# Performance work log

Hardware: AMD Instinct MI355X
Metric: run time of the kernel (lower is better)

Reference implementation:

```python
import jax, jax.numpy as jnp
import numpy as np

B, L, D_MODEL = 2, 1024, 1024
D_STATE, D_CONV, EXPAND = 16, 4, 2
D_INNER = D_MODEL * EXPAND
LN_EPS = 1e-5


def setup_inputs() -> dict:
    key = jax.random.key(0)
    ks = jax.random.split(key, 6)
    g = lambda k, shape, scale: (jax.random.normal(k, shape, jnp.float32) * scale)
    x = jax.random.normal(ks[0], (B, L, D_MODEL), jnp.float32)
    in_proj_w = g(ks[1], (2 * D_INNER, D_MODEL), D_MODEL ** -0.5)
    conv_w = g(ks[2], (D_INNER, D_CONV), D_CONV ** -0.5)   # depthwise kernel
    conv_b = jnp.zeros((D_INNER,), jnp.float32)
    x_proj_w = g(ks[3], (2 * D_STATE + 1, D_INNER), D_INNER ** -0.5)
    A_log = jnp.tile(jnp.log(jnp.arange(1, D_STATE + 1, dtype=jnp.float32)), (D_INNER, 1))
    D_param = jnp.ones((D_INNER,), jnp.float32)
    dt_w = g(ks[4], (D_INNER, 1), 1.0)
    dt_b = jnp.full((D_INNER,), -4.0, jnp.float32)
    out_w = g(ks[5], (D_MODEL, D_INNER), D_INNER ** -0.5)
    ln_g = jnp.ones((D_INNER,), jnp.float32)
    ln_b = jnp.zeros((D_INNER,), jnp.float32)
    return dict(x=x, in_proj_w=in_proj_w, conv_w=conv_w, conv_b=conv_b,
                x_proj_w=x_proj_w, A_log=A_log, D_param=D_param,
                dt_w=dt_w, dt_b=dt_b, out_w=out_w, ln_g=ln_g, ln_b=ln_b)


def _forward(x, in_proj_w, conv_w, conv_b, x_proj_w, A_log, D_param,
             dt_w, dt_b, out_w, ln_g, ln_b):
    Lq = x.shape[1]
    xz = jnp.einsum('bld,ed->ble', x, in_proj_w)            # (B,L,2*Di)
    xb, z = xz[..., :D_INNER], xz[..., D_INNER:]
    # causal depthwise conv1d (pad left d_conv-1, valid conv == torch pad+truncate)
    xpad = jnp.pad(xb, ((0, 0), (D_CONV - 1, 0), (0, 0)))
    xc = conv_b
    for k in range(D_CONV):
        xc = xc + xpad[:, k:k + Lq, :] * conv_w[:, k]
    xb = jax.nn.silu(xc)
    proj = jnp.einsum('bld,ed->ble', xb, x_proj_w)          # (B,L,2N+1)
    dt_in = proj[..., :1]
    Bp = proj[..., 1:1 + D_STATE]                            # (B,L,N)
    Cp = proj[..., 1 + D_STATE:]                             # (B,L,N)
    dt = jax.nn.softplus(dt_in * dt_w[:, 0] + dt_b)          # (B,L,Di)
    A = -jnp.exp(A_log)                                      # (Di,N)
    dA = jnp.exp(dt[..., None] * A)                          # (B,L,Di,N)
    x_scaled = (xb * dt)[..., None] * Bp[..., None, :]       # (B,L,Di,N)
    # linear recurrence h[t] = dA[t]*h[t-1] + x_scaled[t] via associative scan
    def comb(a, b):
        return (a[0] * b[0], b[0] * a[1] + b[1])
    _, h = jax.lax.associative_scan(comb, (dA, x_scaled), axis=1)
    y = jnp.einsum('bldn,bln->bld', h, Cp) + xb * D_param    # (B,L,Di)
    mu = jnp.mean(y, axis=-1, keepdims=True)
    var = jnp.var(y, axis=-1, keepdims=True)
    y = (y - mu) / jnp.sqrt(var + LN_EPS) * ln_g + ln_b
    y = y * jax.nn.silu(z)
    return jnp.einsum('bld,ed->ble', y, out_w)               # (B,L,d_model)


def reference(x, in_proj_w, conv_w, conv_b, x_proj_w, A_log, D_param,
              dt_w, dt_b, out_w, ln_g, ln_b):
    return _forward(x, in_proj_w, conv_w, conv_b, x_proj_w, A_log, D_param,
                    dt_w, dt_b, out_w, ln_g, ln_b)
```

## Files before the change

### kernel.cpp

```cpp
#include <hip/hip_runtime.h>

typedef unsigned short u16;
typedef unsigned int u32;
typedef __bf16 bf16x8 __attribute__((ext_vector_type(8)));
typedef float f32x4 __attribute__((ext_vector_type(4)));

__device__ __forceinline__ float bf2f(u16 b) {
    return __uint_as_float(((u32)b) << 16);
}
__device__ __forceinline__ u16 f2bf(float f) {
    u32 u = __float_as_uint(f);
    return (u16)((u + 0x7fffu + ((u >> 16) & 1u)) >> 16);
}

#define P_CONVW 0
#define P_CONVB 8192
#define P_ALOG  10240
#define P_DPAR  43008
#define P_DTW   45056
#define P_DTB   47104
#define P_LNG   49152
#define P_LNB   51200
#define P_TOTAL 53248

#define CCH 32
#define CT  32
#define CHUNKTOT 2097152
#define PSTRIDE 128

struct ParamPtrs { const void* p[8]; };

__global__ __launch_bounds__(256) void canon_params(ParamPtrs pp, float* __restrict__ dst,
                                                    const u16* __restrict__ dp) {
    const bool isbf = (dp[0] != 0);
    const int i = blockIdx.x * 256 + threadIdx.x;
    int seg, off;
    if (i < P_CONVB)      { seg = 0; off = i; }
    else if (i < P_ALOG)  { seg = 1; off = i - P_CONVB; }
    else if (i < P_DPAR)  { seg = 2; off = i - P_ALOG; }
    else if (i < P_DTW)   { seg = 3; off = i - P_DPAR; }
    else if (i < P_DTB)   { seg = 4; off = i - P_DTW; }
    else if (i < P_LNG)   { seg = 5; off = i - P_DTB; }
    else if (i < P_LNB)   { seg = 6; off = i - P_LNG; }
    else                  { seg = 7; off = i - P_LNB; }
    dst[i] = isbf ? bf2f(((const u16*)pp.p[seg])[off]) : ((const float*)pp.p[seg])[off];
}

#define CV_X   524288
#define CV_W1  1572864
#define CV_TOT 2097152
__global__ __launch_bounds__(256) void canon_multi(const void* __restrict__ sx,
                                                   const void* __restrict__ sw1,
                                                   const void* __restrict__ swo,
                                                   u16* __restrict__ dst,
                                                   const u16* __restrict__ dp) {
    const bool isbf = (dp[0] != 0);
    const int i = blockIdx.x * 256 + threadIdx.x;
    if (i >= CV_TOT) return;
    const void* src;
    int off;
    if (i < CV_X)       { src = sx;  off = i; }
    else if (i < CV_W1) { src = sw1; off = i - CV_X; }
    else                { src = swo; off = i - CV_W1; }
    if (isbf) {
        ((uint2*)dst)[i] = ((const uint2*)src)[off];
    } else {
        const float4 v = ((const float4*)src)[off];
        uint2 o;
        o.x = (u32)f2bf(v.x) | ((u32)f2bf(v.y) << 16);
        o.y = (u32)f2bf(v.z) | ((u32)f2bf(v.w) << 16);
        ((uint2*)dst)[i] = o;
    }
}

__global__ __launch_bounds__(256) void canon_wpad(const void* __restrict__ src,
                                                  u16* __restrict__ dst,
                                                  const u16* __restrict__ dp) {
    const bool isbf = (dp[0] != 0);
    const int i = blockIdx.x * 256 + threadIdx.x;
    const int idx = i * 4;
    const int row = idx >> 11;
    u16 o[4];
#pragma unroll
    for (int q = 0; q < 4; ++q) {
        float v = 0.f;
        if (row < 33)
            v = isbf ? bf2f(((const u16*)src)[idx + q]) : ((const float*)src)[idx + q];
        o[q] = f2bf(v);
    }
    *(uint2*)&dst[idx] = *(uint2*)o;
}

template <bool STORE_F32>
__global__ __launch_bounds__(256) void gemm_bt(const u16* __restrict__ A,
                                               const u16* __restrict__ Bw,
                                               void* __restrict__ C,
                                               int M, int N, int Kseg,
                                               int lda, int ldb) {
    const int bm = blockIdx.x;
    const int bn = blockIdx.y;
    const int kbase = blockIdx.z * Kseg;
    const int tid = threadIdx.x;
    const int lane = tid & 63;
    const int wave = tid >> 6;
    const int wm = wave >> 1, wn = wave & 1;
    const int l16 = lane & 15, quad = lane >> 4;

    __shared__ __align__(16) u16 sA[128 * 32];
    __shared__ __align__(16) u16 sB[128 * 32];

    f32x4 acc[4][4] = {};

    const int rsub = lane >> 2;
    const int csub = (lane & 3) * 8;

    for (int k0 = 0; k0 < Kseg; k0 += 32) {
        const int kc = kbase + k0 + csub;
        __syncthreads();
#pragma unroll
        for (int q = 0; q < 2; ++q) {
            const int g = wave + 4 * q;
            const int row = g * 16 + rsub;
            __builtin_amdgcn_global_load_lds(
                (const u32*)&A[(size_t)(bm * 128 + row) * lda + kc],
                (u32*)&sA[g * 512], 16, 0, 0);
            __builtin_amdgcn_global_load_lds(
                (const u32*)&Bw[(size_t)(bn * 128 + row) * ldb + kc],
                (u32*)&sB[g * 512], 16, 0, 0);
        }
        __syncthreads();

        bf16x8 af[4], bg[4];
#pragma unroll
        for (int t = 0; t < 4; ++t) {
            af[t] = *(const bf16x8*)&sA[(wm * 64 + t * 16 + l16) * 32 + quad * 8];
            bg[t] = *(const bf16x8*)&sB[(wn * 64 + t * 16 + l16) * 32 + quad * 8];
        }
#pragma unroll
        for (int mt = 0; mt < 4; ++mt)
#pragma unroll
            for (int nt = 0; nt < 4; ++nt)
                acc[mt][nt] = __builtin_amdgcn_mfma_f32_16x16x32_bf16(
                    af[mt], bg[nt], acc[mt][nt], 0, 0, 0);
    }

    float* Cf = (float*)C + (size_t)blockIdx.z * M * N;
#pragma unroll
    for (int mt = 0; mt < 4; ++mt) {
#pragma unroll
        for (int r = 0; r < 4; ++r) {
            const int row = bm * 128 + wm * 64 + mt * 16 + quad * 4 + r;
#pragma unroll
            for (int nt = 0; nt < 4; ++nt) {
                const int col = bn * 128 + wn * 64 + nt * 16 + l16;
                if (STORE_F32)
                    Cf[(size_t)row * N + col] = acc[mt][nt][r];
                else
                    ((u16*)C)[(size_t)row * N + col] = f2bf(acc[mt][nt][r]);
            }
        }
    }
}

__global__ __launch_bounds__(256) void reduce_parts(const float* __restrict__ src,
                                                    float* __restrict__ dst,
                                                    int n4, int parts) {
    const int i = blockIdx.x * 256 + threadIdx.x;
    if (i >= n4) return;
    float4 s = ((const float4*)src)[i];
    for (int p = 1; p < parts; ++p) {
        const float4 v = ((const float4*)src)[(size_t)p * n4 + i];
        s.x += v.x; s.y += v.y; s.z += v.z; s.w += v.w;
    }
    ((float4*)dst)[i] = s;
}

__global__ __launch_bounds__(256) void conv_silu(const u16* __restrict__ xz,
                                                 const float* __restrict__ par,
                                                 u16* __restrict__ xb16) {
    const int idx = blockIdx.x * 256 + threadIdx.x;
    const int d = idx & 2047;
    const int bl = idx >> 11;
    const int l = bl & 1023;
    float acc = par[P_CONVB + d];
#pragma unroll
    for (int k = 0; k < 4; ++k) {
        const int ls = l + k - 3;
        if (ls >= 0)
            acc = fmaf(bf2f(xz[(size_t)(bl + (ls - l)) * 4096 + d]),
                       par[P_CONVW + d * 4 + k], acc);
    }
    const float s = acc / (1.f + __expf(-acc));
    xb16[idx] = f2bf(s);
}

__global__ __launch_bounds__(256) void scan_p1(const u16* __restrict__ xb16,
                                               const float* __restrict__ proj,
                                               const float* __restrict__ par,
                                               float* __restrict__ PS) {
    const int d = blockIdx.x * 256 + threadIdx.x;
    const int c = blockIdx.y;
    const int b = blockIdx.z;
    __shared__ float sp[CT][33];
    const size_t row0 = (size_t)b * 1024 + c * CT;
    for (int f = threadIdx.x; f < CT * 33; f += 256) {
        const int i = f / 33, j = f - i * 33;
        sp[i][j] = proj[(row0 + i) * PSTRIDE + j];
    }
    float Aneg[16];
#pragma unroll
    for (int n = 0; n < 16; ++n) Aneg[n] = -__expf(par[P_ALOG + d * 16 + n]);
    const float dtw = par[P_DTW + d], dtb = par[P_DTB + d];
    __syncthreads();

    float h[16] = {}, P[16];
#pragma unroll
    for (int n = 0; n < 16; ++n) P[n] = 1.f;

    float xv = bf2f(xb16[row0 * 2048 + d]);
    for (int i = 0; i < CT; ++i) {
        const float xv_next = (i + 1 < CT) ? bf2f(xb16[(row0 + i + 1) * 2048 + d]) : 0.f;
        const float dtin = sp[i][0];
        const float darg = fmaf(dtin, dtw, dtb);
        const float dt = (darg > 20.f) ? darg : __logf(1.f + __expf(darg));
        const float xdt = xv * dt;
#pragma unroll
        for (int n = 0; n < 16; ++n) {
            const float dA = __expf(dt * Aneg[n]);
            P[n] *= dA;
            h[n] = fmaf(dA, h[n], xdt * sp[i][1 + n]);
        }
        xv = xv_next;
    }
    const size_t base = (((size_t)b * CCH + c) * 16) * 2048 + d;
#pragma unroll
    for (int n = 0; n < 16; ++n) {
        PS[base + (size_t)n * 2048] = P[n];
        PS[CHUNKTOT + base + (size_t)n * 2048] = h[n];
    }
}

__global__ __launch_bounds__(256) void scan_comb(const float* __restrict__ PS,
                                                 float* __restrict__ H) {
    const int t = blockIdx.x * 256 + threadIdx.x;
    const int d = t & 2047;
    const int n = (t >> 11) & 15;
    const int b = t >> 15;
    float h = 0.f;
#pragma unroll
    for (int c = 0; c < CCH; ++c) {
        const size_t idx = (((size_t)b * CCH + c) * 16 + n) * 2048 + d;
        H[idx] = h;
        h = fmaf(PS[idx], h, PS[CHUNKTOT + idx]);
    }
}

__global__ __launch_bounds__(256) void scan_p2(const u16* __restrict__ xb16,
                                               const float* __restrict__ proj,
                                               const float* __restrict__ par,
                                               const float* __restrict__ H,
                                               u16* __restrict__ y) {
    const int d = blockIdx.x * 256 + threadIdx.x;
    const int c = blockIdx.y;
    const int b = blockIdx.z;
    __shared__ float sp[CT][33];
    const size_t row0 = (size_t)b * 1024 + c * CT;
    for (int f = threadIdx.x; f < CT * 33; f += 256) {
        const int i = f / 33, j = f - i * 33;
        sp[i][j] = proj[(row0 + i) * PSTRIDE + j];
    }
    float Aneg[16], h[16];
    const size_t hbase = (((size_t)b * CCH + c) * 16) * 2048 + d;
#pragma unroll
    for (int n = 0; n < 16; ++n) {
        Aneg[n] = -__expf(par[P_ALOG + d * 16 + n]);
        h[n] = H[hbase + (size_t)n * 2048];
    }
    const float dtw = par[P_DTW + d], dtb = par[P_DTB + d];
    const float Dp = par[P_DPAR + d];
    __syncthreads();

    float xv = bf2f(xb16[row0 * 2048 + d]);
    for (int i = 0; i < CT; ++i) {
        const float xv_next = (i + 1 < CT) ? bf2f(xb16[(row0 + i + 1) * 2048 + d]) : 0.f;
        const float dtin = sp[i][0];
        const float darg = fmaf(dtin, dtw, dtb);
        const float dt = (darg > 20.f) ? darg : __logf(1.f + __expf(darg));
        const float xdt = xv * dt;
        float acc = 0.f;
#pragma unroll
        for (int n = 0; n < 16; ++n) {
            const float dA = __expf(dt * Aneg[n]);
            h[n] = fmaf(dA, h[n], xdt * sp[i][1 + n]);
            acc = fmaf(h[n], sp[i][17 + n], acc);
        }
        y[(row0 + i) * 2048 + d] = f2bf(fmaf(xv, Dp, acc));
        xv = xv_next;
    }
}

__global__ __launch_bounds__(256) void ln_silu(const u16* __restrict__ y,
                                               const u16* __restrict__ xz,
                                               const float* __restrict__ par,
                                               u16* __restrict__ yn) {
    const int row = blockIdx.x;
    const int tid = threadIdx.x;
    const int lane = tid & 63, wave = tid >> 6;
    float v[8];
    float s = 0.f, s2 = 0.f;
#pragma unroll
    for (int i = 0; i < 8; ++i) {
        v[i] = bf2f(y[(size_t)row * 2048 + tid + i * 256]);
        s += v[i];
        s2 = fmaf(v[i], v[i], s2);
    }
    s += __shfl_xor(s, 1); s2 += __shfl_xor(s2, 1);
    s += __shfl_xor(s, 2); s2 += __shfl_xor(s2, 2);
    s += __shfl_xor(s, 4); s2 += __shfl_xor(s2, 4);
    s += __shfl_xor(s, 8); s2 += __shfl_xor(s2, 8);
    s += __shfl_xor(s, 16); s2 += __shfl_xor(s2, 16);
    s += __shfl_xor(s, 32); s2 += __shfl_xor(s2, 32);
    __shared__ float rs[4], rs2[4];
    if (lane == 0) { rs[wave] = s; rs2[wave] = s2; }
    __syncthreads();
    const float ts = rs[0] + rs[1] + rs[2] + rs[3];
    const float ts2 = rs2[0] + rs2[1] + rs2[2] + rs2[3];
    const float mu = ts * (1.f / 2048.f);
    const float var = ts2 * (1.f / 2048.f) - mu * mu;
    const float rstd = rsqrtf(var + 1e-5f);
#pragma unroll
    for (int i = 0; i < 8; ++i) {
        const int d = tid + i * 256;
        float t = (v[i] - mu) * rstd * par[P_LNG + d] + par[P_LNB + d];
        const float z = bf2f(xz[(size_t)row * 4096 + 2048 + d]);
        t *= z / (1.f + __expf(-z));
        yn[(size_t)row * 2048 + d] = f2bf(t);
    }
}

extern "C" void kernel_launch(void* const* d_in, const int* in_sizes, int n_in,
                              void* d_out, int out_size, void* d_ws, size_t ws_size,
                              hipStream_t stream) {
    const void* x         = d_in[0];
    const void* in_proj_w = d_in[1];
    const void* conv_w    = d_in[2];
    const void* conv_b    = d_in[3];
    const void* x_proj_w  = d_in[4];
    const void* A_log     = d_in[5];
    const void* D_param   = d_in[6];
    const void* dt_w      = d_in[7];
    const void* dt_b      = d_in[8];
    const void* out_w     = d_in[9];
    const void* ln_g      = d_in[10];
    const void* ln_b      = d_in[11];
    const u16* dp = (const u16*)D_param;

    float* cpar = (float*)d_ws;
    u16* cx     = (u16*)(cpar + P_TOTAL);
    u16* cw1    = cx + 2097152;
    u16* cwo    = cw1 + 4194304;
    u16* xz     = cwo + 2097152;
    u16* xb16   = xz + 8388608;
    u16* y      = xb16 + 4194304;
    u16* wpad   = y + 4194304;
    float* proj = (float*)(wpad + 262144);
    float* PS   = proj + 262144;
    float* H    = PS + 2 * CHUNKTOT;
    float* xpart = (float*)cx;
    float* gpart = PS;
    u16* yn      = xb16;

    ParamPtrs pp;
    pp.p[0] = conv_w; pp.p[1] = conv_b; pp.p[2] = A_log; pp.p[3] = D_param;
    pp.p[4] = dt_w;   pp.p[5] = dt_b;   pp.p[6] = ln_g;  pp.p[7] = ln_b;
    canon_params<<<P_TOTAL / 256, 256, 0, stream>>>(pp, cpar, dp);
    canon_multi<<<CV_TOT / 256, 256, 0, stream>>>(x, in_proj_w, out_w, cx, dp);
    canon_wpad<<<256, 256, 0, stream>>>(x_proj_w, wpad, dp);

    gemm_bt<false><<<dim3(16, 32, 1), 256, 0, stream>>>(cx, cw1, xz, 2048, 4096, 1024, 1024, 1024);
    conv_silu<<<16384, 256, 0, stream>>>(xz, cpar, xb16);
    gemm_bt<true><<<dim3(16, 1, 8), 256, 0, stream>>>(xb16, wpad, xpart, 2048, 128, 256, 2048, 2048);
    reduce_parts<<<256, 256, 0, stream>>>(xpart, proj, 65536, 8);
    scan_p1<<<dim3(8, CCH, 2), 256, 0, stream>>>(xb16, proj, cpar, PS);
    scan_comb<<<256, 256, 0, stream>>>(PS, H);
    scan_p2<<<dim3(8, CCH, 2), 256, 0, stream>>>(xb16, proj, cpar, H, y);
    ln_silu<<<2048, 256, 0, stream>>>(y, xz, cpar, yn);
    gemm_bt<true><<<dim3(16, 8, 2), 256, 0, stream>>>(yn, cwo, gpart, 2048, 1024, 1024, 2048, 2048);
    reduce_parts<<<2048, 256, 0, stream>>>(gpart, (float*)d_out, 524288, 2);
}
```

Measured before the change: 256.3 us.

## Merge canon kernels, replace split-K reductions with atomics, vectorize conv and layernorm

Folds the three input-canonicalisation kernels into one launch, which also zero-fills the projection buffer and the output. Both split-K GEMMs now accumulate through float atomic adds, which removes the two reduce_parts passes and their partial-sum buffers. The conv+SiLU and LN+SiLU kernels are rewritten to process 8 channels per thread with 128-bit loads and stores. This cuts launches and memory traffic, but atomic accumulation makes the floating-point summation order nondeterministic.

New measurement: 255.4 us. Within noise of the previous version (-0.3%).

```diff
diff --git a/kernel.cpp b/kernel.cpp
--- a/kernel.cpp
+++ b/kernel.cpp
@@ -4,6 +4,7 @@
 typedef unsigned int u32;
 typedef __bf16 bf16x8 __attribute__((ext_vector_type(8)));
 typedef float f32x4 __attribute__((ext_vector_type(4)));
+typedef unsigned short ushort8 __attribute__((ext_vector_type(8)));
 
 __device__ __forceinline__ float bf2f(u16 b) {
     return __uint_as_float(((u32)b) << 16);
@@ -28,70 +29,76 @@
 #define CHUNKTOT 2097152
 #define PSTRIDE 128
 
-struct ParamPtrs { const void* p[8]; };
-
-__global__ __launch_bounds__(256) void canon_params(ParamPtrs pp, float* __restrict__ dst,
-                                                    const u16* __restrict__ dp) {
-    const bool isbf = (dp[0] != 0);
-    const int i = blockIdx.x * 256 + threadIdx.x;
-    int seg, off;
-    if (i < P_CONVB)      { seg = 0; off = i; }
-    else if (i < P_ALOG)  { seg = 1; off = i - P_CONVB; }
-    else if (i < P_DPAR)  { seg = 2; off = i - P_ALOG; }
-    else if (i < P_DTW)   { seg = 3; off = i - P_DPAR; }
-    else if (i < P_DTB)   { seg = 4; off = i - P_DTW; }
-    else if (i < P_LNG)   { seg = 5; off = i - P_DTB; }
-    else if (i < P_LNB)   { seg = 6; off = i - P_LNG; }
-    else                  { seg = 7; off = i - P_LNB; }
-    dst[i] = isbf ? bf2f(((const u16*)pp.p[seg])[off]) : ((const float*)pp.p[seg])[off];
-}
-
 #define CV_X   524288
 #define CV_W1  1572864
 #define CV_TOT 2097152
-__global__ __launch_bounds__(256) void canon_multi(const void* __restrict__ sx,
-                                                   const void* __restrict__ sw1,
-                                                   const void* __restrict__ swo,
-                                                   u16* __restrict__ dst,
-                                                   const u16* __restrict__ dp) {
+
+struct ParamPtrs { const void* p[8]; };
+
+__global__ __launch_bounds__(256) void canon_all(ParamPtrs pp, float* __restrict__ cpar,
+                                                 const void* __restrict__ sx,
+                                                 const void* __restrict__ sw1,
+                                                 const void* __restrict__ swo,
+                                                 u16* __restrict__ cx,
+                                                 const void* __restrict__ sxp,
+                                                 u16* __restrict__ wpad,
+                                                 float* __restrict__ proj,
+                                                 float* __restrict__ dout,
+                                                 const u16* __restrict__ dp) {
     const bool isbf = (dp[0] != 0);
-    const int i = blockIdx.x * 256 + threadIdx.x;
-    if (i >= CV_TOT) return;
-    const void* src;
-    int off;
-    if (i < CV_X)       { src = sx;  off = i; }
-    else if (i < CV_W1) { src = sw1; off = i - CV_X; }
-    else                { src = swo; off = i - CV_W1; }
-    if (isbf) {
-        ((uint2*)dst)[i] = ((const uint2*)src)[off];
+    const int blk = blockIdx.x;
+    const int tid = threadIdx.x;
+    if (blk < 8192) {
+        const int i = blk * 256 + tid;
+        const void* src;
+        int off;
+        if (i < CV_X)       { src = sx;  off = i; }
+        else if (i < CV_W1) { src = sw1; off = i - CV_X; }
+        else                { src = swo; off = i - CV_W1; }
+        if (isbf) {
+            ((uint2*)cx)[i] = ((const uint2*)src)[off];
+        } else {
+            const float4 v = ((const float4*)src)[off];
+            uint2 o;
+            o.x = (u32)f2bf(v.x) | ((u32)f2bf(v.y) << 16);
+            o.y = (u32)f2bf(v.z) | ((u32)f2bf(v.w) << 16);
+            ((uint2*)cx)[i] = o;
+        }
+    } else if (blk < 8400) {
+        const int i = (blk - 8192) * 256 + tid;
+        int seg, off;
+        if (i < P_CONVB)      { seg = 0; off = i; }
+        else if (i < P_ALOG)  { seg = 1; off = i - P_CONVB; }
+        else if (i < P_DPAR)  { seg = 2; off = i - P_ALOG; }
+        else if (i < P_DTW)   { seg = 3; off = i - P_DPAR; }
+        else if (i < P_DTB)   { seg = 4; off = i - P_DTW; }
+        else if (i < P_LNG)   { seg = 5; off = i - P_DTB; }
+        else if (i < P_LNB)   { seg = 6; off = i - P_LNG; }
+        else                  { seg = 7; off = i - P_LNB; }
+        cpar[i] = isbf ? bf2f(((const u16*)pp.p[seg])[off]) : ((const float*)pp.p[seg])[off];
+    } else if (blk < 8656) {
+        const int i = (blk - 8400) * 256 + tid;
+        const int idx = i * 4;
+        const int row = idx >> 11;
+        u16 o[4];
+#pragma unroll
+        for (int q = 0; q < 4; ++q) {
+            float v = 0.f;
+            if (row < 33)
+                v = isbf ? bf2f(((const u16*)sxp)[idx + q]) : ((const float*)sxp)[idx + q];
+            o[q] = f2bf(v);
+        }
+        *(uint2*)&wpad[idx] = *(uint2*)o;
+    } else if (blk < 8912) {
+        const int i = (blk - 8656) * 256 + tid;
+        ((float4*)proj)[i] = make_float4(0.f, 0.f, 0.f, 0.f);
     } else {
-        const float4 v = ((const float4*)src)[off];
-        uint2 o;
-        o.x = (u32)f2bf(v.x) | ((u32)f2bf(v.y) << 16);
-        o.y = (u32)f2bf(v.z) | ((u32)f2bf(v.w) << 16);
-        ((uint2*)dst)[i] = o;
-    }
-}
-
-__global__ __launch_bounds__(256) void canon_wpad(const void* __restrict__ src,
-                                                  u16* __restrict__ dst,
-                                                  const u16* __restrict__ dp) {
-    const bool isbf = (dp[0] != 0);
-    const int i = blockIdx.x * 256 + threadIdx.x;
-    const int idx = i * 4;
-    const int row = idx >> 11;
-    u16 o[4];
-#pragma unroll
-    for (int q = 0; q < 4; ++q) {
-        float v = 0.f;
-        if (row < 33)
-            v = isbf ? bf2f(((const u16*)src)[idx + q]) : ((const float*)src)[idx + q];
-        o[q] = f2bf(v);
-    }
-    *(uint2*)&dst[idx] = *(uint2*)o;
-}
-
-template <bool STORE_F32>
+        const int i = (blk - 8912) * 256 + tid;
+        ((float4*)dout)[i] = make_float4(0.f, 0.f, 0.f, 0.f);
+    }
+}
+
+template <int MODE>
 __global__ __launch_bounds__(256) void gemm_bt(const u16* __restrict__ A,
                                                const u16* __restrict__ Bw,
                                                void* __restrict__ C,
@@ -144,7 +151,7 @@
                     af[mt], bg[nt], acc[mt][nt], 0, 0, 0);
     }
 
-    float* Cf = (float*)C + (size_t)blockIdx.z * M * N;
+    float* Cf = (float*)C + (MODE == 1 ? (size_t)blockIdx.z * M * N : (size_t)0);
 #pragma unroll
     for (int mt = 0; mt < 4; ++mt) {
 #pragma unroll
@@ -153,45 +160,56 @@
 #pragma unroll
             for (int nt = 0; nt < 4; ++nt) {
                 const int col = bn * 128 + wn * 64 + nt * 16 + l16;
-                if (STORE_F32)
+                if (MODE == 0)
+                    ((u16*)C)[(size_t)row * N + col] = f2bf(acc[mt][nt][r]);
+                else if (MODE == 1)
                     Cf[(size_t)row * N + col] = acc[mt][nt][r];
                 else
-                    ((u16*)C)[(size_t)row * N + col] = f2bf(acc[mt][nt][r]);
+                    unsafeAtomicAdd(&Cf[(size_t)row * N + col], acc[mt][nt][r]);
             }
         }
     }
-}
-
-__global__ __launch_bounds__(256) void reduce_parts(const float* __restrict__ src,
-                                                    float* __restrict__ dst,
-                                                    int n4, int parts) {
-    const int i = blockIdx.x * 256 + threadIdx.x;
-    if (i >= n4) return;
-    float4 s = ((const float4*)src)[i];
-    for (int p = 1; p < parts; ++p) {
-        const float4 v = ((const float4*)src)[(size_t)p * n4 + i];
-        s.x += v.x; s.y += v.y; s.z += v.z; s.w += v.w;
-    }
-    ((float4*)dst)[i] = s;
 }
 
 __global__ __launch_bounds__(256) void conv_silu(const u16* __restrict__ xz,
                                                  const float* __restrict__ par,
                                                  u16* __restrict__ xb16) {
     const int idx = blockIdx.x * 256 + threadIdx.x;
-    const int d = idx & 2047;
-    const int bl = idx >> 11;
+    const int d8 = idx & 255;
+    const int bl = idx >> 8;
     const int l = bl & 1023;
-    float acc = par[P_CONVB + d];
+    const int d0 = d8 * 8;
+
+    float acc[8];
+    {
+        const float4 b0 = *(const float4*)&par[P_CONVB + d0];
+        const float4 b1 = *(const float4*)&par[P_CONVB + d0 + 4];
+        acc[0] = b0.x; acc[1] = b0.y; acc[2] = b0.z; acc[3] = b0.w;
+        acc[4] = b1.x; acc[5] = b1.y; acc[6] = b1.z; acc[7] = b1.w;
+    }
+    float warr[8][4];
+#pragma unroll
+    for (int q = 0; q < 8; ++q) {
+        const float4 w = *(const float4*)&par[P_CONVW + (d0 + q) * 4];
+        warr[q][0] = w.x; warr[q][1] = w.y; warr[q][2] = w.z; warr[q][3] = w.w;
+    }
 #pragma unroll
     for (int k = 0; k < 4; ++k) {
         const int ls = l + k - 3;
-        if (ls >= 0)
-            acc = fmaf(bf2f(xz[(size_t)(bl + (ls - l)) * 4096 + d]),
-                       par[P_CONVW + d * 4 + k], acc);
-    }
-    const float s = acc / (1.f + __expf(-acc));
-    xb16[idx] = f2bf(s);
+        if (ls >= 0) {
+            const ushort8 xv = *(const ushort8*)&xz[(size_t)(bl + k - 3) * 4096 + d0];
+#pragma unroll
+            for (int q = 0; q < 8; ++q)
+                acc[q] = fmaf(bf2f(xv[q]), warr[q][k], acc[q]);
+        }
+    }
+    u16 o[8];
+#pragma unroll
+    for (int q = 0; q < 8; ++q) {
+        const float s = acc[q] / (1.f + __expf(-acc[q]));
+        o[q] = f2bf(s);
+    }
+    *(uint4*)&xb16[(size_t)bl * 2048 + d0] = *(uint4*)o;
 }
 
 __global__ __launch_bounds__(256) void scan_p1(const u16* __restrict__ xb16,
@@ -306,11 +324,13 @@
     const int row = blockIdx.x;
     const int tid = threadIdx.x;
     const int lane = tid & 63, wave = tid >> 6;
+    const int d0 = tid * 8;
+    const ushort8 vy = *(const ushort8*)&y[(size_t)row * 2048 + d0];
     float v[8];
     float s = 0.f, s2 = 0.f;
 #pragma unroll
     for (int i = 0; i < 8; ++i) {
-        v[i] = bf2f(y[(size_t)row * 2048 + tid + i * 256]);
+        v[i] = bf2f(vy[i]);
         s += v[i];
         s2 = fmaf(v[i], v[i], s2);
     }
@@ -328,14 +348,28 @@
     const float mu = ts * (1.f / 2048.f);
     const float var = ts2 * (1.f / 2048.f) - mu * mu;
     const float rstd = rsqrtf(var + 1e-5f);
+
+    const ushort8 vz = *(const ushort8*)&xz[(size_t)row * 4096 + 2048 + d0];
+    float g[8], bb[8];
+    {
+        const float4 g0 = *(const float4*)&par[P_LNG + d0];
+        const float4 g1 = *(const float4*)&par[P_LNG + d0 + 4];
+        g[0] = g0.x; g[1] = g0.y; g[2] = g0.z; g[3] = g0.w;
+        g[4] = g1.x; g[5] = g1.y; g[6] = g1.z; g[7] = g1.w;
+        const float4 b0 = *(const float4*)&par[P_LNB + d0];
+        const float4 b1 = *(const float4*)&par[P_LNB + d0 + 4];
+        bb[0] = b0.x; bb[1] = b0.y; bb[2] = b0.z; bb[3] = b0.w;
+        bb[4] = b1.x; bb[5] = b1.y; bb[6] = b1.z; bb[7] = b1.w;
+    }
+    u16 o[8];
 #pragma unroll
     for (int i = 0; i < 8; ++i) {
-        const int d = tid + i * 256;
-        float t = (v[i] - mu) * rstd * par[P_LNG + d] + par[P_LNB + d];
-        const float z = bf2f(xz[(size_t)row * 4096 + 2048 + d]);
+        float t = (v[i] - mu) * rstd * g[i] + bb[i];
+        const float z = bf2f(vz[i]);
         t *= z / (1.f + __expf(-z));
-        yn[(size_t)row * 2048 + d] = f2bf(t);
-    }
+        o[i] = f2bf(t);
+    }
+    *(uint4*)&yn[(size_t)row * 2048 + d0] = *(uint4*)o;
 }
 
 extern "C" void kernel_launch(void* const* d_in, const int* in_sizes, int n_in,
@@ -366,25 +400,20 @@
     float* proj = (float*)(wpad + 262144);
     float* PS   = proj + 262144;
     float* H    = PS + 2 * CHUNKTOT;
-    float* xpart = (float*)cx;
-    float* gpart = PS;
-    u16* yn      = xb16;
+    u16* yn     = xb16;
 
     ParamPtrs pp;
     pp.p[0] = conv_w; pp.p[1] = conv_b; pp.p[2] = A_log; pp.p[3] = D_param;
     pp.p[4] = dt_w;   pp.p[5] = dt_b;   pp.p[6] = ln_g;  pp.p[7] = ln_b;
-    canon_params<<<P_TOTAL / 256, 256, 0, stream>>>(pp, cpar, dp);
-    canon_multi<<<CV_TOT / 256, 256, 0, stream>>>(x, in_proj_w, out_w, cx, dp);
-    canon_wpad<<<256, 256, 0, stream>>>(x_proj_w, wpad, dp);
-
-    gemm_bt<false><<<dim3(16, 32, 1), 256, 0, stream>>>(cx, cw1, xz, 2048, 4096, 1024, 1024, 1024);
-    conv_silu<<<16384, 256, 0, stream>>>(xz, cpar, xb16);
-    gemm_bt<true><<<dim3(16, 1, 8), 256, 0, stream>>>(xb16, wpad, xpart, 2048, 128, 256, 2048, 2048);
-    reduce_parts<<<256, 256, 0, stream>>>(xpart, proj, 65536, 8);
+    canon_all<<<10960, 256, 0, stream>>>(pp, cpar, x, in_proj_w, out_w, cx,
+                                         x_proj_w, wpad, proj, (float*)d_out, dp);
+
+    gemm_bt<0><<<dim3(16, 32, 1), 256, 0, stream>>>(cx, cw1, xz, 2048, 4096, 1024, 1024, 1024);
+    conv_silu<<<2048, 256, 0, stream>>>(xz, cpar, xb16);
+    gemm_bt<2><<<dim3(16, 1, 8), 256, 0, stream>>>(xb16, wpad, proj, 2048, 128, 256, 2048, 2048);
     scan_p1<<<dim3(8, CCH, 2), 256, 0, stream>>>(xb16, proj, cpar, PS);
     scan_comb<<<256, 256, 0, stream>>>(PS, H);
     scan_p2<<<dim3(8, CCH, 2), 256, 0, stream>>>(xb16, proj, cpar, H, y);
     ln_silu<<<2048, 256, 0, stream>>>(y, xz, cpar, yn);
-    gemm_bt<true><<<dim3(16, 8, 2), 256, 0, stream>>>(yn, cwo, gpart, 2048, 1024, 1024, 2048, 2048);
-    reduce_parts<<<2048, 256, 0, stream>>>(gpart, (float*)d_out, 524288, 2);
-}
+    gemm_bt<2><<<dim3(16, 8, 2), 256, 0, stream>>>(yn, cwo, (float*)d_out, 2048, 1024, 1024, 2048, 2048);
+}
```
